# Kernel optimization log

Hardware: AMD Instinct MI355X
Metric: run time of the kernel (lower is better)

## Reference

```python
import jax, jax.numpy as jnp
import numpy as np

N_GRID = 64
DX = 1.0 / N_GRID
INV_DX = float(N_GRID)
DT = 5e-4
BOUND = 3
GRAVITY = np.array([0.0, -9.8, 0.0], dtype=np.float32)
P_VOL = (DX * 0.5) ** 3          # particle volume (NCLaw convention)
P_RHO = 1000.0
P_MASS = P_VOL * P_RHO
N_PART = 500000


def setup_inputs() -> dict:
    key = jax.random.key(0)
    k1, k2, k3, k4, k5 = jax.random.split(key, 5)
    # particles inside the domain, away from the boundary
    x = 0.2 + 0.6 * jax.random.uniform(k1, (N_PART, 3), dtype=jnp.float32)
    v = 0.1 * jax.random.normal(k2, (N_PART, 3), dtype=jnp.float32)
    C = 0.1 * jax.random.normal(k3, (N_PART, 3, 3), dtype=jnp.float32)
    F = jnp.eye(3, dtype=jnp.float32)[None] + 0.01 * jax.random.normal(k4, (N_PART, 3, 3), dtype=jnp.float32)
    s = jax.random.normal(k5, (N_PART, 3, 3), dtype=jnp.float32)
    stress = 100.0 * 0.5 * (s + jnp.swapaxes(s, -1, -2))  # symmetric Cauchy stress
    return {"x": x, "v": v, "C": C, "F": F, "stress": stress}


def _mpm_step(x, v, C, F, stress):
    # quadratic B-spline stencil
    base = jnp.floor(x * INV_DX - 0.5).astype(jnp.int32)        # [N,3]
    fx = x * INV_DX - base.astype(x.dtype)                      # [N,3]
    # weights per offset (0,1,2) per axis -> [N,3(off),3(dim)]
    w = jnp.stack([0.5 * (1.5 - fx) ** 2,
                   0.75 - (fx - 1.0) ** 2,
                   0.5 * (fx - 0.5) ** 2], axis=1)
    # MLS-MPM fused stress + APIC affine term
    affine = stress * (-DT * P_VOL * 4.0 * INV_DX * INV_DX) + P_MASS * C  # [N,3,3]

    offs = jnp.stack(jnp.meshgrid(jnp.arange(3), jnp.arange(3), jnp.arange(3),
                                  indexing='ij'), axis=-1).reshape(27, 3)  # [27,3]
    wi = w[:, offs[:, 0], 0] * w[:, offs[:, 1], 1] * w[:, offs[:, 2], 2]   # [N,27]
    dpos = (offs[None, :, :].astype(x.dtype) - fx[:, None, :]) * DX        # [N,27,3] physical
    mom = P_MASS * v[:, None, :] + jnp.einsum('nij,nkj->nki', affine, dpos)  # [N,27,3]

    idx = base[:, None, :] + offs[None, :, :]                               # [N,27,3]
    flat = (idx[..., 0] * N_GRID + idx[..., 1]) * N_GRID + idx[..., 2]      # [N,27]
    flat_r = flat.reshape(-1)
    G = N_GRID ** 3
    grid_mv = jnp.zeros((G, 3), dtype=x.dtype).at[flat_r].add((wi[..., None] * mom).reshape(-1, 3))
    grid_m = jnp.zeros((G,), dtype=x.dtype).at[flat_r].add((wi * P_MASS).reshape(-1))

    has_mass = grid_m > 0.0
    grid_v = jnp.where(has_mass[:, None], grid_mv / jnp.maximum(grid_m, 1e-10)[:, None], 0.0)
    grid_v = jnp.where(has_mass[:, None], grid_v + DT * jnp.asarray(GRAVITY, x.dtype), 0.0)

    # sticky-ish boundary: zero inflow velocity near walls
    gi = jnp.arange(G)
    ijk = jnp.stack([gi // (N_GRID * N_GRID), (gi // N_GRID) % N_GRID, gi % N_GRID], axis=-1)
    low = (ijk < BOUND) & (grid_v < 0.0)
    high = (ijk >= N_GRID - BOUND) & (grid_v > 0.0)
    grid_v = jnp.where(low | high, 0.0, grid_v)

    # G2P gather
    gv = grid_v[flat]                                              # [N,27,3]
    v_next = jnp.einsum('nk,nkd->nd', wi, gv)                      # [N,3]
    C_next = (4.0 * INV_DX * INV_DX) * jnp.einsum('nk,nki,nkj->nij', wi, gv, dpos)
    x_next = x + DT * v_next
    F_next = jnp.einsum('nij,njk->nik', jnp.eye(3, dtype=x.dtype)[None] + DT * C_next, F)
    return x_next, v_next, C_next, F_next


def reference(x, v, C, F, stress):
    return _mpm_step(x, v, C, F, stress)
```

## Files before the change

### kernel.cpp

```cpp
#include <hip/hip_runtime.h>
#include <math.h>

namespace {
constexpr int   NG    = 64;
constexpr int   GC    = NG * NG * NG;
constexpr int   BOUND = 3;
constexpr float DXf    = 1.0f / 64.0f;
constexpr float INV_DX = 64.0f;
constexpr float DTf    = 5e-4f;
constexpr double P_VOL_D = (0.5 / 64.0) * (0.5 / 64.0) * (0.5 / 64.0);
constexpr float P_MASS_F = (float)(P_VOL_D * 1000.0);
constexpr float AFFINE_SCALE = (float)(-5e-4 * P_VOL_D * 4.0 * 64.0 * 64.0);
constexpr float D_INV  = 4.0f * 64.0f * 64.0f;
constexpr float GRAV_Y = -9.8f;

__device__ __forceinline__ void atom_add_f32(float* p, float v) {
    unsafeAtomicAdd(p, v);
}

__device__ __forceinline__ void weights_of(float fx0, float fx1, float fx2, float w[3][3]) {
    w[0][0] = 0.5f*(1.5f-fx0)*(1.5f-fx0); w[0][1] = 0.5f*(1.5f-fx1)*(1.5f-fx1); w[0][2] = 0.5f*(1.5f-fx2)*(1.5f-fx2);
    w[1][0] = 0.75f-(fx0-1.0f)*(fx0-1.0f); w[1][1] = 0.75f-(fx1-1.0f)*(fx1-1.0f); w[1][2] = 0.75f-(fx2-1.0f)*(fx2-1.0f);
    w[2][0] = 0.5f*(fx0-0.5f)*(fx0-0.5f); w[2][1] = 0.5f*(fx1-0.5f)*(fx1-0.5f); w[2][2] = 0.5f*(fx2-0.5f)*(fx2-0.5f);
}

__device__ __forceinline__ float bspline_w(float u) {
    float au = fabsf(u);
    float a  = 1.5f - au;
    float w  = (au < 0.5f) ? (0.75f - u * u) : (0.5f * a * a);
    return (au < 1.5f) ? w : 0.f;
}
}

__global__ __launch_bounds__(256) void count_kernel(const float* __restrict__ x,
                                                    int* __restrict__ cnt, int n)
{
    int p = blockIdx.x * 256 + threadIdx.x;
    if (p >= n) return;
    float u0 = x[3*p] * INV_DX, u1 = x[3*p+1] * INV_DX, u2 = x[3*p+2] * INV_DX;
    int b0 = (int)floorf(u0 - 0.5f), b1 = (int)floorf(u1 - 0.5f), b2 = (int)floorf(u2 - 0.5f);
    if ((unsigned)b0 >= 64u || (unsigned)b1 >= 64u || (unsigned)b2 >= 64u) return;
    atomicAdd(&cnt[((b0 << 6) + b1) * 64 + b2], 1);
}

__global__ __launch_bounds__(256) void scanA(const int* __restrict__ cnt,
                                             int* __restrict__ start,
                                             int* __restrict__ aux)
{
    __shared__ int sh[256];
    int tid = threadIdx.x;
    int i = blockIdx.x * 256 + tid;
    int v = cnt[i];
    sh[tid] = v;
    __syncthreads();
    for (int off = 1; off < 256; off <<= 1) {
        int t = (tid >= off) ? sh[tid - off] : 0;
        __syncthreads();
        sh[tid] += t;
        __syncthreads();
    }
    start[i] = sh[tid] - v;
    if (tid == 255) aux[blockIdx.x] = sh[255];
}

__global__ __launch_bounds__(256) void scanB(int* __restrict__ aux,
                                             int* __restrict__ start)
{
    __shared__ int partial[256];
    int tid = threadIdx.x;
    int local[4];
    int s = 0;
#pragma unroll
    for (int i = 0; i < 4; ++i) { local[i] = s; s += aux[tid * 4 + i]; }
    partial[tid] = s;
    __syncthreads();
    for (int off = 1; off < 256; off <<= 1) {
        int v = (tid >= off) ? partial[tid - off] : 0;
        __syncthreads();
        partial[tid] += v;
        __syncthreads();
    }
    int base = (tid > 0) ? partial[tid - 1] : 0;
#pragma unroll
    for (int i = 0; i < 4; ++i) aux[tid * 4 + i] = base + local[i];
    if (tid == 255) start[GC] = partial[255];
}

__global__ __launch_bounds__(256) void scanC(int* __restrict__ start,
                                             const int* __restrict__ aux,
                                             int* __restrict__ cursor)
{
    int i = blockIdx.x * 256 + threadIdx.x;
    int v = start[i] + aux[blockIdx.x];
    start[i] = v;
    cursor[i] = v;
}

__global__ __launch_bounds__(256) void reorder_kernel(const float* __restrict__ x,
                                                      const float* __restrict__ v,
                                                      const float* __restrict__ C,
                                                      const float* __restrict__ st,
                                                      int* __restrict__ cursor,
                                                      float4* __restrict__ payload, int n)
{
    int p = blockIdx.x * 256 + threadIdx.x;
    if (p >= n) return;

    float u0 = x[3*p] * INV_DX, u1 = x[3*p+1] * INV_DX, u2 = x[3*p+2] * INV_DX;
    int b0 = (int)floorf(u0 - 0.5f), b1 = (int)floorf(u1 - 0.5f), b2 = (int)floorf(u2 - 0.5f);
    if ((unsigned)b0 >= 64u || (unsigned)b1 >= 64u || (unsigned)b2 >= 64u) return;

    float aff[9];
#pragma unroll
    for (int i = 0; i < 9; ++i)
        aff[i] = st[9*p + i] * AFFINE_SCALE + P_MASS_F * C[9*p + i];
    float mv0 = P_MASS_F * v[3*p], mv1 = P_MASS_F * v[3*p+1], mv2 = P_MASS_F * v[3*p+2];

    int pos = atomicAdd(&cursor[((b0 << 6) + b1) * 64 + b2], 1);

    float4* dst = payload + 4 * (size_t)pos;
    dst[0] = make_float4(aff[0], aff[1], aff[2], aff[3]);
    dst[1] = make_float4(aff[4], aff[5], aff[6], aff[7]);
    dst[2] = make_float4(aff[8], mv0, mv1, mv2);
    dst[3] = make_float4(u0, u1, u2, 0.f);
}

__global__ __launch_bounds__(256) void p2g_cell8(const float4* __restrict__ payload,
                                                 const int* __restrict__ start,
                                                 float* __restrict__ grid)
{
    int w   = blockIdx.x;
    int xcd = w & 7, j = w >> 3;
    int cj  = j >> 4, oj = j & 15;
    int r   = cj * 128 + xcd * 16 + oj;

    int row01 = r >> 1;
    int g0 = row01 >> 6, g1 = row01 & 63;
    int tid = threadIdx.x;
    int cl = tid >> 3, q = tid & 7;
    int g2 = ((r & 1) << 5) + cl;
    float fg0 = (float)g0, fg1 = (float)g1, fg2 = (float)g2;

    float acc0 = 0.f, acc1 = 0.f, acc2 = 0.f, acc3 = 0.f;
    int klo = (g2 >= 2) ? g2 - 2 : 0;

#define P2G_SEG(SS, QOFF, STRIDE)                                            \
    {   int o0 = (SS) / 3, o1 = (SS) % 3;                                    \
        int b0 = g0 - o0, b1 = g1 - o1;                                      \
        if ((unsigned)b0 < 64u && (unsigned)b1 < 64u) {                      \
            int rowp = ((b0 << 6) + b1) << 6;                                \
            int s = start[rowp + klo] + (QOFF);                              \
            int e = start[rowp + g2 + 1];                                    \
            float4 c0, c1, c2, c3;                                           \
            if (s < e) {                                                     \
                const float4* rp = payload + 4 * (size_t)s;                  \
                c0 = rp[0]; c1 = rp[1]; c2 = rp[2]; c3 = rp[3];              \
            }                                                                \
            for (int idx = s; idx < e; ) {                                   \
                float4 r0 = c0, r1 = c1, r2 = c2, r3 = c3;                   \
                idx += (STRIDE);                                             \
                if (idx < e) {                                               \
                    const float4* rp = payload + 4 * (size_t)idx;            \
                    c0 = rp[0]; c1 = rp[1]; c2 = rp[2]; c3 = rp[3];          \
                }                                                            \
                float u0 = r3.x - fg0, u1 = r3.y - fg1, u2 = r3.z - fg2;     \
                float wq = bspline_w(u0) * bspline_w(u1) * bspline_w(u2);    \
                float dp0 = -u0 * DXf, dp1 = -u1 * DXf, dp2 = -u2 * DXf;     \
                acc0 += wq * (r2.y + r0.x * dp0 + r0.y * dp1 + r0.z * dp2);  \
                acc1 += wq * (r2.z + r0.w * dp0 + r1.x * dp1 + r1.y * dp2);  \
                acc2 += wq * (r2.w + r1.z * dp0 + r1.w * dp1 + r2.x * dp2);  \
                acc3 += wq * P_MASS_F;                                       \
            }                                                                \
        }                                                                    \
    }

    P2G_SEG(q, 0, 1)
    P2G_SEG(8, q, 8)
#undef P2G_SEG

    acc0 += __shfl_down(acc0, 1); acc1 += __shfl_down(acc1, 1);
    acc2 += __shfl_down(acc2, 1); acc3 += __shfl_down(acc3, 1);
    acc0 += __shfl_down(acc0, 2); acc1 += __shfl_down(acc1, 2);
    acc2 += __shfl_down(acc2, 2); acc3 += __shfl_down(acc3, 2);
    acc0 += __shfl_down(acc0, 4); acc1 += __shfl_down(acc1, 4);
    acc2 += __shfl_down(acc2, 4); acc3 += __shfl_down(acc3, 4);

    if (q == 0) {
        float v0 = 0.f, v1 = 0.f, v2 = 0.f;
        if (acc3 > 0.f) {
            float mm = fmaxf(acc3, 1e-10f);
            v0 = acc0 / mm;
            v1 = acc1 / mm + DTf * GRAV_Y;
            v2 = acc2 / mm;
        }
        if ((g0 < BOUND && v0 < 0.f) || (g0 >= NG - BOUND && v0 > 0.f)) v0 = 0.f;
        if ((g1 < BOUND && v1 < 0.f) || (g1 >= NG - BOUND && v1 > 0.f)) v1 = 0.f;
        if ((g2 < BOUND && v2 < 0.f) || (g2 >= NG - BOUND && v2 > 0.f)) v2 = 0.f;
        ((float4*)grid)[row01 * 64 + g2] = make_float4(v0, v1, v2, acc3);
    }
}

__global__ __launch_bounds__(256) void p2g_naive(const float* __restrict__ x,
                                                 const float* __restrict__ v,
                                                 const float* __restrict__ C,
                                                 const float* __restrict__ st,
                                                 float* __restrict__ grid, int n)
{
    int p = blockIdx.x * 256 + threadIdx.x;
    if (p >= n) return;

    float xp0 = x[3*p], xp1 = x[3*p+1], xp2 = x[3*p+2];
    float u0 = xp0 * INV_DX, u1 = xp1 * INV_DX, u2 = xp2 * INV_DX;
    float b0f = floorf(u0 - 0.5f), b1f = floorf(u1 - 0.5f), b2f = floorf(u2 - 0.5f);
    int base0 = (int)b0f, base1 = (int)b1f, base2 = (int)b2f;
    float fx0 = u0 - b0f, fx1 = u1 - b1f, fx2 = u2 - b2f;

    float w[3][3];
    weights_of(fx0, fx1, fx2, w);

    float aff[3][3];
#pragma unroll
    for (int i = 0; i < 3; ++i)
#pragma unroll
        for (int j = 0; j < 3; ++j)
            aff[i][j] = st[9*p + 3*i + j] * AFFINE_SCALE + P_MASS_F * C[9*p + 3*i + j];

    float mv0 = P_MASS_F * v[3*p], mv1 = P_MASS_F * v[3*p+1], mv2 = P_MASS_F * v[3*p+2];

#pragma unroll
    for (int i = 0; i < 3; ++i) {
        float dp0 = ((float)i - fx0) * DXf;
#pragma unroll
        for (int j = 0; j < 3; ++j) {
            float dp1 = ((float)j - fx1) * DXf;
            float wij = w[i][0] * w[j][1];
            float m0 = mv0 + aff[0][0]*dp0 + aff[0][1]*dp1;
            float m1 = mv1 + aff[1][0]*dp0 + aff[1][1]*dp1;
            float m2 = mv2 + aff[2][0]*dp0 + aff[2][1]*dp1;
            int cellij = ((base0 + i) * NG + (base1 + j)) * NG + base2;
#pragma unroll
            for (int k = 0; k < 3; ++k) {
                float dp2 = ((float)k - fx2) * DXf;
                float wi = wij * w[k][2];
                float* cptr = grid + 4 * (cellij + k);
                atom_add_f32(cptr + 0, wi * (m0 + aff[0][2]*dp2));
                atom_add_f32(cptr + 1, wi * (m1 + aff[1][2]*dp2));
                atom_add_f32(cptr + 2, wi * (m2 + aff[2][2]*dp2));
                atom_add_f32(cptr + 3, wi * P_MASS_F);
            }
        }
    }
}

__global__ __launch_bounds__(256) void grid_kernel(float* __restrict__ grid)
{
    int g = blockIdx.x * 256 + threadIdx.x;
    if (g >= GC) return;
    float4 val = ((const float4*)grid)[g];
    float m = val.w;
    float v0 = 0.f, v1 = 0.f, v2 = 0.f;
    if (m > 0.f) {
        float mm = fmaxf(m, 1e-10f);
        v0 = val.x / mm;
        v1 = val.y / mm + DTf * GRAV_Y;
        v2 = val.z / mm;
    }
    int ci = g >> 12, cj = (g >> 6) & 63, ck = g & 63;
    if ((ci < BOUND && v0 < 0.f) || (ci >= NG - BOUND && v0 > 0.f)) v0 = 0.f;
    if ((cj < BOUND && v1 < 0.f) || (cj >= NG - BOUND && v1 > 0.f)) v1 = 0.f;
    if ((ck < BOUND && v2 < 0.f) || (ck >= NG - BOUND && v2 > 0.f)) v2 = 0.f;
    ((float4*)grid)[g] = make_float4(v0, v1, v2, m);
}

__global__ __launch_bounds__(256) void g2p_kernel(const float* __restrict__ x,
                                                  const float* __restrict__ F,
                                                  const float* __restrict__ grid,
                                                  float* __restrict__ out_x,
                                                  float* __restrict__ out_v,
                                                  float* __restrict__ out_C,
                                                  float* __restrict__ out_F,
                                                  int n)
{
    int p = blockIdx.x * 256 + threadIdx.x;
    if (p >= n) return;

    float xp0 = x[3*p], xp1 = x[3*p+1], xp2 = x[3*p+2];
    float t0 = xp0 * INV_DX, t1 = xp1 * INV_DX, t2 = xp2 * INV_DX;
    float b0 = floorf(t0 - 0.5f), b1 = floorf(t1 - 0.5f), b2 = floorf(t2 - 0.5f);
    int   base0 = (int)b0, base1 = (int)b1, base2 = (int)b2;
    float fx0 = t0 - b0, fx1 = t1 - b1, fx2 = t2 - b2;

    float w[3][3];
    weights_of(fx0, fx1, fx2, w);

    float vn0 = 0.f, vn1 = 0.f, vn2 = 0.f;
    float Cn[3][3] = {};

#pragma unroll
    for (int i = 0; i < 3; ++i) {
        float dp0 = ((float)i - fx0) * DXf;
#pragma unroll
        for (int j = 0; j < 3; ++j) {
            float dp1 = ((float)j - fx1) * DXf;
            float wij = w[i][0] * w[j][1];
            int cellij = ((base0 + i) * NG + (base1 + j)) * NG + base2;
#pragma unroll
            for (int k = 0; k < 3; ++k) {
                float dp2 = ((float)k - fx2) * DXf;
                float wi = wij * w[k][2];
                float4 gv = ((const float4*)grid)[cellij + k];
                vn0 += wi * gv.x; vn1 += wi * gv.y; vn2 += wi * gv.z;
                float wx = wi * gv.x, wy = wi * gv.y, wz = wi * gv.z;
                Cn[0][0] += wx * dp0; Cn[0][1] += wx * dp1; Cn[0][2] += wx * dp2;
                Cn[1][0] += wy * dp0; Cn[1][1] += wy * dp1; Cn[1][2] += wy * dp2;
                Cn[2][0] += wz * dp0; Cn[2][1] += wz * dp1; Cn[2][2] += wz * dp2;
            }
        }
    }

#pragma unroll
    for (int i = 0; i < 3; ++i)
#pragma unroll
        for (int j = 0; j < 3; ++j)
            Cn[i][j] *= D_INV;

    out_x[3*p]   = xp0 + DTf * vn0;
    out_x[3*p+1] = xp1 + DTf * vn1;
    out_x[3*p+2] = xp2 + DTf * vn2;
    out_v[3*p]   = vn0; out_v[3*p+1] = vn1; out_v[3*p+2] = vn2;

    float Fp[3][3];
#pragma unroll
    for (int i = 0; i < 3; ++i)
#pragma unroll
        for (int j = 0; j < 3; ++j)
            Fp[i][j] = F[9*p + 3*i + j];

#pragma unroll
    for (int i = 0; i < 3; ++i) {
#pragma unroll
        for (int k = 0; k < 3; ++k) {
            float acc = Cn[i][0]*Fp[0][k] + Cn[i][1]*Fp[1][k] + Cn[i][2]*Fp[2][k];
            out_F[9*p + 3*i + k] = Fp[i][k] + DTf * acc;
            out_C[9*p + 3*i + k] = Cn[i][k];
        }
    }
}

extern "C" void kernel_launch(void* const* d_in, const int* in_sizes, int n_in,
                              void* d_out, int out_size, void* d_ws, size_t ws_size,
                              hipStream_t stream)
{
    const float* x  = (const float*)d_in[0];
    const float* v  = (const float*)d_in[1];
    const float* C  = (const float*)d_in[2];
    const float* F  = (const float*)d_in[3];
    const float* st = (const float*)d_in[4];
    int n = in_sizes[0] / 3;

    const size_t grid_bytes = (size_t)GC * 4 * sizeof(float);
    const size_t tab_ints   = 3 * (size_t)GC + 1 + 1024;
    const bool   use_tiled  = ws_size >= grid_bytes &&
                              (size_t)out_size >= 22 * (size_t)n + tab_ints;

    float* grid = (float*)d_ws;

    float* out  = (float*)d_out;
    float* out_x = out;
    float* out_v = out + 3 * (size_t)n;
    float* out_C = out + 6 * (size_t)n;
    float* out_F = out + 15 * (size_t)n;
    float4* payload = (float4*)(out + 6 * (size_t)n);
    int* tab    = (int*)(out + 22 * (size_t)n);
    int* cnt    = tab;
    int* tstart = tab + GC;
    int* cursor = tab + 2 * GC + 1;
    int* aux    = tab + 3 * GC + 1;

    int pblocks = (n + 255) / 256;

    if (use_tiled) {
        hipMemsetAsync(cnt, 0, (size_t)GC * sizeof(int), stream);
        count_kernel<<<pblocks, 256, 0, stream>>>(x, cnt, n);
        scanA<<<GC / 256, 256, 0, stream>>>(cnt, tstart, aux);
        scanB<<<1, 256, 0, stream>>>(aux, tstart);
        scanC<<<GC / 256, 256, 0, stream>>>(tstart, aux, cursor);
        reorder_kernel<<<pblocks, 256, 0, stream>>>(x, v, C, st, cursor, payload, n);
        p2g_cell8<<<GC / 32, 256, 0, stream>>>(payload, tstart, grid);
    } else {
        hipMemsetAsync(grid, 0, grid_bytes, stream);
        p2g_naive<<<pblocks, 256, 0, stream>>>(x, v, C, st, grid, n);
        grid_kernel<<<GC / 256, 256, 0, stream>>>(grid);
    }

    g2p_kernel<<<pblocks, 256, 0, stream>>>(x, F, grid, out_x, out_v, out_C, out_F, n);
}
```

Before: 390.7 us.

## Gather P2G over 4-cell strips per thread to reuse particle loads

Each group of 8 lanes now accumulates four consecutive z-cells instead of one. Every loaded particle is applied to all four cells, and the x/y weight and momentum partials are shared across them. Blocks shrink to 64 threads while the grid size stays the same. This cuts redundant payload reads and weight math by widening each thread's z-range from 3 to 6 cells. The cost is 16 accumulators per thread, more shuffles, and some wasted work on particles outside a given cell's stencil.

```diff
diff --git a/kernel.cpp b/kernel.cpp
--- a/kernel.cpp
+++ b/kernel.cpp
@@ -125,9 +125,9 @@
     dst[3] = make_float4(u0, u1, u2, 0.f);
 }
 
-__global__ __launch_bounds__(256) void p2g_cell8(const float4* __restrict__ payload,
-                                                 const int* __restrict__ start,
-                                                 float* __restrict__ grid)
+__global__ __launch_bounds__(64) void p2g_strip(const float4* __restrict__ payload,
+                                                const int* __restrict__ start,
+                                                float* __restrict__ grid)
 {
     int w   = blockIdx.x;
     int xcd = w & 7, j = w >> 3;
@@ -137,12 +137,27 @@
     int row01 = r >> 1;
     int g0 = row01 >> 6, g1 = row01 & 63;
     int tid = threadIdx.x;
-    int cl = tid >> 3, q = tid & 7;
-    int g2 = ((r & 1) << 5) + cl;
-    float fg0 = (float)g0, fg1 = (float)g1, fg2 = (float)g2;
-
-    float acc0 = 0.f, acc1 = 0.f, acc2 = 0.f, acc3 = 0.f;
-    int klo = (g2 >= 2) ? g2 - 2 : 0;
+    int sl = tid >> 3, q = tid & 7;
+    int g2b = ((r & 1) << 5) + sl * 4;
+    float fg0 = (float)g0, fg1 = (float)g1, fg2b = (float)g2b;
+
+    float a00=0.f,a01=0.f,a02=0.f,a03=0.f;
+    float a10=0.f,a11=0.f,a12=0.f,a13=0.f;
+    float a20=0.f,a21=0.f,a22=0.f,a23=0.f;
+    float a30=0.f,a31=0.f,a32=0.f,a33=0.f;
+
+    int klo = (g2b >= 2) ? g2b - 2 : 0;
+    int khi = (g2b + 3 <= 63) ? g2b + 3 : 63;
+
+#define P2G_CELL(CC, A0, A1, A2, A3)                                         \
+    {   float u2  = r3.z - (fg2b + (float)CC);                               \
+        float w2  = bspline_w(u2);                                           \
+        float wq  = w01 * w2;                                                \
+        float dp2 = -u2 * DXf;                                               \
+        A0 += wq * (m0 + r0.z * dp2);                                        \
+        A1 += wq * (m1 + r1.y * dp2);                                        \
+        A2 += wq * (m2 + r2.x * dp2);                                        \
+        A3 += wq * P_MASS_F; }
 
 #define P2G_SEG(SS, QOFF, STRIDE)                                            \
     {   int o0 = (SS) / 3, o1 = (SS) % 3;                                    \
@@ -150,7 +165,7 @@
         if ((unsigned)b0 < 64u && (unsigned)b1 < 64u) {                      \
             int rowp = ((b0 << 6) + b1) << 6;                                \
             int s = start[rowp + klo] + (QOFF);                              \
-            int e = start[rowp + g2 + 1];                                    \
+            int e = start[rowp + khi + 1];                                   \
             float4 c0, c1, c2, c3;                                           \
             if (s < e) {                                                     \
                 const float4* rp = payload + 4 * (size_t)s;                  \
@@ -163,13 +178,16 @@
                     const float4* rp = payload + 4 * (size_t)idx;            \
                     c0 = rp[0]; c1 = rp[1]; c2 = rp[2]; c3 = rp[3];          \
                 }                                                            \
-                float u0 = r3.x - fg0, u1 = r3.y - fg1, u2 = r3.z - fg2;     \
-                float wq = bspline_w(u0) * bspline_w(u1) * bspline_w(u2);    \
-                float dp0 = -u0 * DXf, dp1 = -u1 * DXf, dp2 = -u2 * DXf;     \
-                acc0 += wq * (r2.y + r0.x * dp0 + r0.y * dp1 + r0.z * dp2);  \
-                acc1 += wq * (r2.z + r0.w * dp0 + r1.x * dp1 + r1.y * dp2);  \
-                acc2 += wq * (r2.w + r1.z * dp0 + r1.w * dp1 + r2.x * dp2);  \
-                acc3 += wq * P_MASS_F;                                       \
+                float u0  = r3.x - fg0, u1 = r3.y - fg1;                     \
+                float w01 = bspline_w(u0) * bspline_w(u1);                   \
+                float dp0 = -u0 * DXf, dp1 = -u1 * DXf;                      \
+                float m0 = r2.y + r0.x * dp0 + r0.y * dp1;                   \
+                float m1 = r2.z + r0.w * dp0 + r1.x * dp1;                   \
+                float m2 = r2.w + r1.z * dp0 + r1.w * dp1;                   \
+                P2G_CELL(0, a00, a01, a02, a03)                              \
+                P2G_CELL(1, a10, a11, a12, a13)                              \
+                P2G_CELL(2, a20, a21, a22, a23)                              \
+                P2G_CELL(3, a30, a31, a32, a33)                              \
             }                                                                \
         }                                                                    \
     }
@@ -177,26 +195,39 @@
     P2G_SEG(q, 0, 1)
     P2G_SEG(8, q, 8)
 #undef P2G_SEG
-
-    acc0 += __shfl_down(acc0, 1); acc1 += __shfl_down(acc1, 1);
-    acc2 += __shfl_down(acc2, 1); acc3 += __shfl_down(acc3, 1);
-    acc0 += __shfl_down(acc0, 2); acc1 += __shfl_down(acc1, 2);
-    acc2 += __shfl_down(acc2, 2); acc3 += __shfl_down(acc3, 2);
-    acc0 += __shfl_down(acc0, 4); acc1 += __shfl_down(acc1, 4);
-    acc2 += __shfl_down(acc2, 4); acc3 += __shfl_down(acc3, 4);
+#undef P2G_CELL
+
+#define RED(OFF)                                                             \
+    a00 += __shfl_down(a00, OFF); a01 += __shfl_down(a01, OFF);              \
+    a02 += __shfl_down(a02, OFF); a03 += __shfl_down(a03, OFF);              \
+    a10 += __shfl_down(a10, OFF); a11 += __shfl_down(a11, OFF);              \
+    a12 += __shfl_down(a12, OFF); a13 += __shfl_down(a13, OFF);              \
+    a20 += __shfl_down(a20, OFF); a21 += __shfl_down(a21, OFF);              \
+    a22 += __shfl_down(a22, OFF); a23 += __shfl_down(a23, OFF);              \
+    a30 += __shfl_down(a30, OFF); a31 += __shfl_down(a31, OFF);              \
+    a32 += __shfl_down(a32, OFF); a33 += __shfl_down(a33, OFF);
+    RED(1) RED(2) RED(4)
+#undef RED
 
     if (q == 0) {
-        float v0 = 0.f, v1 = 0.f, v2 = 0.f;
-        if (acc3 > 0.f) {
-            float mm = fmaxf(acc3, 1e-10f);
-            v0 = acc0 / mm;
-            v1 = acc1 / mm + DTf * GRAV_Y;
-            v2 = acc2 / mm;
-        }
-        if ((g0 < BOUND && v0 < 0.f) || (g0 >= NG - BOUND && v0 > 0.f)) v0 = 0.f;
-        if ((g1 < BOUND && v1 < 0.f) || (g1 >= NG - BOUND && v1 > 0.f)) v1 = 0.f;
-        if ((g2 < BOUND && v2 < 0.f) || (g2 >= NG - BOUND && v2 > 0.f)) v2 = 0.f;
-        ((float4*)grid)[row01 * 64 + g2] = make_float4(v0, v1, v2, acc3);
+#define STORE_CELL(CC, A0, A1, A2, A3)                                       \
+    {   int g2 = g2b + CC;                                                   \
+        float v0 = 0.f, v1 = 0.f, v2 = 0.f;                                  \
+        if (A3 > 0.f) {                                                      \
+            float mm = fmaxf(A3, 1e-10f);                                    \
+            v0 = A0 / mm;                                                    \
+            v1 = A1 / mm + DTf * GRAV_Y;                                     \
+            v2 = A2 / mm;                                                    \
+        }                                                                    \
+        if ((g0 < BOUND && v0 < 0.f) || (g0 >= NG - BOUND && v0 > 0.f)) v0 = 0.f; \
+        if ((g1 < BOUND && v1 < 0.f) || (g1 >= NG - BOUND && v1 > 0.f)) v1 = 0.f; \
+        if ((g2 < BOUND && v2 < 0.f) || (g2 >= NG - BOUND && v2 > 0.f)) v2 = 0.f; \
+        ((float4*)grid)[row01 * 64 + g2] = make_float4(v0, v1, v2, A3); }
+        STORE_CELL(0, a00, a01, a02, a03)
+        STORE_CELL(1, a10, a11, a12, a13)
+        STORE_CELL(2, a20, a21, a22, a23)
+        STORE_CELL(3, a30, a31, a32, a33)
+#undef STORE_CELL
     }
 }
 
@@ -386,7 +417,7 @@
         scanB<<<1, 256, 0, stream>>>(aux, tstart);
         scanC<<<GC / 256, 256, 0, stream>>>(tstart, aux, cursor);
         reorder_kernel<<<pblocks, 256, 0, stream>>>(x, v, C, st, cursor, payload, n);
-        p2g_cell8<<<GC / 32, 256, 0, stream>>>(payload, tstart, grid);
+        p2g_strip<<<GC / 32, 64, 0, stream>>>(payload, tstart, grid);
     } else {
         hipMemsetAsync(grid, 0, grid_bytes, stream);
         p2g_naive<<<pblocks, 256, 0, stream>>>(x, v, C, st, grid, n);
```

Result: faster. 338.7 us (-13.3%).
